# Optimization experiments

Hardware: AMD Instinct MI355X
Metric: run time of the kernel (lower is better)

Reference implementation:

```python
import jax, jax.numpy as jnp
import numpy as np

B, T, N_EMBD, HEAD = 4, 4096, 1024, 64


def setup_inputs() -> dict:
    key = jax.random.key(0)
    kx, kk, kq, kv = jax.random.split(key, 4)
    x = jax.random.normal(kx, (B, T, N_EMBD), dtype=jnp.float32)
    s = 1.0 / np.sqrt(N_EMBD)  # init scale so activations stay O(1)
    Wk = jax.random.normal(kk, (N_EMBD, HEAD), dtype=jnp.float32) * s
    Wq = jax.random.normal(kq, (N_EMBD, HEAD), dtype=jnp.float32) * s
    Wv = jax.random.normal(kv, (N_EMBD, HEAD), dtype=jnp.float32) * s
    return {"x": x, "Wk": Wk, "Wq": Wq, "Wv": Wv}


def reference(x, Wk, Wq, Wv):
    Bd, Td, C = x.shape
    k = jnp.einsum('btc,ch->bth', x, Wk)
    q = jnp.einsum('btc,ch->bth', x, Wq)
    v = jnp.einsum('btc,ch->bth', x, Wv)
    # scores scaled by C**-0.5 where C = n_embd (as in the source, not head_size)
    w = jnp.einsum('bth,bsh->bts', q, k) * (C ** -0.5)
    causal = jnp.tril(jnp.ones((Td, Td), dtype=bool))  # [T, T]
    w = jnp.where(causal, w, -jnp.inf)
    w = jax.nn.softmax(w, axis=-1)
    out = jnp.einsum('bts,bsh->bth', w, v)  # [B, T, head_size]
    return out
```

## Files before the change

### kernel.cpp

```cpp
#include <hip/hip_runtime.h>
#include <cmath>

#define NB 4
#define NT 4096
#define NC 1024
#define NH 64
#define SCALE 0.03125f
#define MFIX 3.0f
#define LOG2E 1.4426950408889634f
#define NSPLIT 12

typedef __attribute__((ext_vector_type(8))) short v8s;
typedef __attribute__((ext_vector_type(4))) float f32x4;

static __device__ __forceinline__ ushort f2bf(float x) {
    union { float f; uint u; } c; c.f = x;
    return (ushort)((c.u + 0x7FFF + ((c.u >> 16) & 1)) >> 16);
}
static __device__ __forceinline__ float bf2f(ushort h) {
    union { uint u; float f; } c; c.u = (uint)h << 16;
    return c.f;
}

__global__ __launch_bounds__(256) void prep_kernel(
    const float* __restrict__ Wk, const float* __restrict__ Wq,
    const float* __restrict__ Wv, ushort* __restrict__ Wb)
{
    const int g    = blockIdx.x * 256 + threadIdx.x;
    const int lane = g & 63;
    const int kc   = (g >> 6) & 31;
    const int nt   = g >> 11;
    const int n    = nt * 16 + (lane & 15);
    const float* W = (n < 64) ? Wq : (n < 128) ? Wk : Wv;
    const int col  = n & 63;
    const int k0   = kc * 32 + ((lane >> 4) << 3);
    ushort t8[8];
    #pragma unroll
    for (int j = 0; j < 8; ++j)
        t8[j] = f2bf(W[(k0 + j) * 64 + col]);
    *(uint4*)(Wb + (size_t)g * 8) = *(const uint4*)t8;
}

#define PPAD 72

__global__ __launch_bounds__(256) void proj_kernel(
    const float* __restrict__ x, const ushort* __restrict__ Wb,
    ushort* __restrict__ q, ushort* __restrict__ kpack, ushort* __restrict__ vpack)
{
    __shared__ __align__(16) ushort As[2][32 * PPAD];
    __shared__ __align__(16) ushort Cs[32][200];

    const int tid  = threadIdx.x;
    const int w    = tid >> 6;
    const int lane = tid & 63;
    const int ln   = lane & 15;
    const int quad = lane >> 4;
    const long r0  = (long)blockIdx.x * 32;

    const int arow = tid >> 3, acol = (tid & 7) * 8;
    const float* xs = x + (r0 + arow) * NC + acol;

    const ushort* wb0 = Wb + (size_t)(w * 3 + 0) * 16384 + lane * 8;
    const ushort* wb1 = Wb + (size_t)(w * 3 + 1) * 16384 + lane * 8;
    const ushort* wb2 = Wb + (size_t)(w * 3 + 2) * 16384 + lane * 8;

    f32x4 acc[2][3];
    #pragma unroll
    for (int s = 0; s < 2; ++s)
        #pragma unroll
        for (int nt = 0; nt < 3; ++nt) acc[s][nt] = (f32x4){0.f,0.f,0.f,0.f};

    float4 f0 = *(const float4*)(xs);
    float4 f1 = *(const float4*)(xs + 4);
    v8s b[3][2];
    b[0][0] = *(const v8s*)(wb0);       b[0][1] = *(const v8s*)(wb0 + 512);
    b[1][0] = *(const v8s*)(wb1);       b[1][1] = *(const v8s*)(wb1 + 512);
    b[2][0] = *(const v8s*)(wb2);       b[2][1] = *(const v8s*)(wb2 + 512);
    {
        ushort t8[8] = { f2bf(f0.x), f2bf(f0.y), f2bf(f0.z), f2bf(f0.w),
                         f2bf(f1.x), f2bf(f1.y), f2bf(f1.z), f2bf(f1.w) };
        *(uint4*)(&As[0][arow * PPAD + acol]) = *(const uint4*)t8;
    }
    __syncthreads();

    int buf = 0;
    #pragma unroll
    for (int it = 0; it < 16; ++it) {
        float4 g0, g1;
        v8s nb[3][2];
        if (it < 15) {
            const int k1 = (it + 1) * 64;
            g0 = *(const float4*)(xs + k1);
            g1 = *(const float4*)(xs + k1 + 4);
            const int off = (it + 1) * 1024;
            nb[0][0] = *(const v8s*)(wb0 + off); nb[0][1] = *(const v8s*)(wb0 + off + 512);
            nb[1][0] = *(const v8s*)(wb1 + off); nb[1][1] = *(const v8s*)(wb1 + off + 512);
            nb[2][0] = *(const v8s*)(wb2 + off); nb[2][1] = *(const v8s*)(wb2 + off + 512);
        }

        #pragma unroll
        for (int s = 0; s < 2; ++s) {
            const ushort* ap = &As[buf][(s * 16 + ln) * PPAD + quad * 8];
            v8s a0 = *(const v8s*)(ap);
            v8s a1 = *(const v8s*)(ap + 32);
            #pragma unroll
            for (int nt = 0; nt < 3; ++nt) {
                acc[s][nt] = __builtin_amdgcn_mfma_f32_16x16x32_bf16(a0, b[nt][0], acc[s][nt], 0, 0, 0);
                acc[s][nt] = __builtin_amdgcn_mfma_f32_16x16x32_bf16(a1, b[nt][1], acc[s][nt], 0, 0, 0);
            }
        }

        if (it < 15) {
            ushort t8[8] = { f2bf(g0.x), f2bf(g0.y), f2bf(g0.z), f2bf(g0.w),
                             f2bf(g1.x), f2bf(g1.y), f2bf(g1.z), f2bf(g1.w) };
            *(uint4*)(&As[buf ^ 1][arow * PPAD + acol]) = *(const uint4*)t8;
            #pragma unroll
            for (int nt = 0; nt < 3; ++nt) {
                b[nt][0] = nb[nt][0];
                b[nt][1] = nb[nt][1];
            }
        }
        __syncthreads();
        buf ^= 1;
    }

    #pragma unroll
    for (int s = 0; s < 2; ++s)
        #pragma unroll
        for (int nt = 0; nt < 3; ++nt)
            #pragma unroll
            for (int r = 0; r < 4; ++r)
                Cs[s * 16 + quad * 4 + r][(w * 3 + nt) * 16 + ln] = f2bf(acc[s][nt][r]);
    __syncthreads();

    const int b_blk = (int)(r0 >> 12);
    const int t_loc = (int)(r0 & 4095);
    const int kt    = t_loc >> 6;
    const int tk0   = (t_loc >> 4) & 3;
    const int kcb   = (t_loc >> 5) & 1;

    {
        const int orow = tid >> 3, oseg = (tid & 7) * 8;
        uint4 u0 = *(const uint4*)(&Cs[orow][oseg]);
        *(uint4*)(q + (r0 + orow) * NH + oseg) = u0;
    }
    {
        const int tk_loc = tid >> 7, kc = (tid >> 6) & 1, lp = tid & 63;
        const int lnp = lp & 15, qdp = lp >> 4;
        uint4 kk = *(const uint4*)(&Cs[tk_loc * 16 + lnp][64 + kc * 32 + qdp * 8]);
        size_t fid = ((size_t)(b_blk * 64 + kt) * 4 + tk0 + tk_loc) * 2 + kc;
        *(uint4*)(kpack + fid * 512 + lp * 8) = kk;
    }
    {
        const int td = tid >> 6, lp = tid & 63;
        const int lnp = lp & 15, qdp = lp >> 4;
        ushort t8[8];
        #pragma unroll
        for (int j = 0; j < 8; ++j)
            t8[j] = Cs[qdp * 8 + j][128 + td * 16 + lnp];
        size_t fid = ((size_t)(b_blk * 64 + kt) * 2 + kcb) * 4 + td;
        *(uint4*)(vpack + fid * 512 + lp * 8) = *(const uint4*)t8;
    }
}

#define LPAD 72

__global__ __launch_bounds__(256) void attn_kernel(
    const ushort* __restrict__ q, const ushort* __restrict__ kpack,
    const ushort* __restrict__ vpack, ushort* __restrict__ Op,
    float* __restrict__ Lp)
{
    __shared__ __align__(16) ushort Ps[4][32 * LPAD];

    const int id = blockIdx.x;
    const int qt = 31 - (id / 48);
    const int c  = (id % 48) >> 2;
    const int b  = id & 3;
    const int q0 = qt * 128;

    const int tid  = threadIdx.x;
    const int w    = tid >> 6;
    const int lane = tid & 63;
    const int ln   = lane & 15;
    const int quad = lane >> 4;
    const int qw0  = q0 + w * 32;

    const ushort* qb  = q + (size_t)b * NT * NH;
    const ushort* kpb = kpack + (size_t)b * 64 * 8 * 512 + lane * 8;
    const ushort* vpb = vpack + (size_t)b * 64 * 8 * 512 + lane * 8;

    v8s qf[2][2];
    #pragma unroll
    for (int s = 0; s < 2; ++s) {
        const ushort* qp = qb + (size_t)(qw0 + s * 16 + ln) * NH + quad * 8;
        qf[s][0] = *(const v8s*)(qp);
        qf[s][1] = *(const v8s*)(qp + 32);
    }

    f32x4 o[2][4];
    #pragma unroll
    for (int s = 0; s < 2; ++s)
        #pragma unroll
        for (int td = 0; td < 4; ++td) o[s][td] = (f32x4){0.f,0.f,0.f,0.f};
    float l[2][4] = {};

    const int nkt   = 2 * qt + 2;
    const int cs    = (nkt + NSPLIT - 1) / NSPLIT;
    const int kt_lo = c * cs;
    const int kt_hi = min(nkt, kt_lo + cs);

    ushort* Pw = &Ps[w][0];

    for (int kt = kt_lo; kt < kt_hi; ++kt) {
        const ushort* kfb = kpb + (size_t)kt * 8 * 512;
        const ushort* vfb = vpb + (size_t)kt * 8 * 512;

        #pragma unroll
        for (int tk = 0; tk < 4; ++tk) {
            v8s kf0 = *(const v8s*)(kfb + (tk * 2 + 0) * 512);
            v8s kf1 = *(const v8s*)(kfb + (tk * 2 + 1) * 512);
            const int sg = kt * 64 + tk * 16 + ln;
            #pragma unroll
            for (int s = 0; s < 2; ++s) {
                f32x4 acc = (f32x4){0.f,0.f,0.f,0.f};
                acc = __builtin_amdgcn_mfma_f32_16x16x32_bf16(qf[s][0], kf0, acc, 0, 0, 0);
                acc = __builtin_amdgcn_mfma_f32_16x16x32_bf16(qf[s][1], kf1, acc, 0, 0, 0);
                const bool needmask = (kt * 64 + 63) > (qw0 + s * 16);
                #pragma unroll
                for (int r = 0; r < 4; ++r) {
                    float e = fmaf(acc[r], SCALE * LOG2E, -MFIX * LOG2E);
                    if (needmask) {
                        int qg = qw0 + s * 16 + quad * 4 + r;
                        if (sg > qg) e = -1e30f;
                    }
                    float p = __builtin_amdgcn_exp2f(e);
                    l[s][r] += p;
                    Pw[(s * 16 + quad * 4 + r) * LPAD + tk * 16 + ln] = f2bf(p);
                }
            }
        }

        #pragma unroll
        for (int kc = 0; kc < 2; ++kc) {
            v8s vf[4];
            #pragma unroll
            for (int td = 0; td < 4; ++td)
                vf[td] = *(const v8s*)(vfb + (kc * 4 + td) * 512);
            #pragma unroll
            for (int s = 0; s < 2; ++s) {
                v8s pf = *(const v8s*)(&Pw[(s * 16 + ln) * LPAD + kc * 32 + quad * 8]);
                #pragma unroll
                for (int td = 0; td < 4; ++td)
                    o[s][td] = __builtin_amdgcn_mfma_f32_16x16x32_bf16(pf, vf[td], o[s][td], 0, 0, 0);
            }
        }
    }

    float lsum[2][4];
    #pragma unroll
    for (int s = 0; s < 2; ++s)
        #pragma unroll
        for (int r = 0; r < 4; ++r) {
            float x_ = l[s][r];
            x_ += __shfl_xor(x_, 1);
            x_ += __shfl_xor(x_, 2);
            x_ += __shfl_xor(x_, 4);
            x_ += __shfl_xor(x_, 8);
            lsum[s][r] = x_;
        }

    ushort* opc = Op + (size_t)c * NB * NT * NH + (size_t)b * NT * NH;
    float*  lpc = Lp + (size_t)c * NB * NT + (size_t)b * NT;
    #pragma unroll
    for (int s = 0; s < 2; ++s)
        #pragma unroll
        for (int r = 0; r < 4; ++r) {
            const int t = qw0 + s * 16 + quad * 4 + r;
            #pragma unroll
            for (int td = 0; td < 4; ++td)
                opc[(size_t)t * NH + td * 16 + ln] = f2bf(o[s][td][r]);
            if (ln == r) lpc[t] = lsum[s][r];
        }
}

__global__ __launch_bounds__(256) void combine_kernel(
    const ushort* __restrict__ Op, const float* __restrict__ Lp,
    float* __restrict__ out)
{
    const size_t g4 = (size_t)blockIdx.x * 256 + threadIdx.x;
    const size_t h0 = (g4 & 15) * 4;
    const size_t bq = g4 >> 4;
    const size_t QN = (size_t)NB * NT;
    const size_t ON = QN * NH;
    float L = 0.f;
    float o0 = 0.f, o1 = 0.f, o2 = 0.f, o3 = 0.f;
    #pragma unroll
    for (int c = 0; c < NSPLIT; ++c) {
        L += Lp[(size_t)c * QN + bq];
        ushort4 u = *(const ushort4*)(Op + (size_t)c * ON + bq * NH + h0);
        o0 += bf2f(u.x); o1 += bf2f(u.y); o2 += bf2f(u.z); o3 += bf2f(u.w);
    }
    const float inv = 1.f / L;
    float4 r = { o0 * inv, o1 * inv, o2 * inv, o3 * inv };
    *(float4*)(out + bq * NH + h0) = r;
}

extern "C" void kernel_launch(void* const* d_in, const int* in_sizes, int n_in,
                              void* d_out, int out_size, void* d_ws, size_t ws_size,
                              hipStream_t stream)
{
    const float* x  = (const float*)d_in[0];
    const float* Wk = (const float*)d_in[1];
    const float* Wq = (const float*)d_in[2];
    const float* Wv = (const float*)d_in[3];
    float* out = (float*)d_out;

    char* wsb = (char*)d_ws;
    const size_t QE = (size_t)NB * NT * NH;
    ushort* qw    = (ushort*)wsb;
    ushort* kpack = qw + QE;
    ushort* vpack = kpack + QE;
    ushort* Wb    = vpack + QE;
    ushort* Op    = (ushort*)(wsb + (8u << 20));
    float*  Lp    = (float*)(wsb + (40u << 20));

    prep_kernel<<<96, 256, 0, stream>>>(Wk, Wq, Wv, Wb);
    proj_kernel<<<NB * NT / 32, 256, 0, stream>>>(x, Wb, qw, kpack, vpack);
    attn_kernel<<<32 * NSPLIT * NB, 256, 0, stream>>>(qw, kpack, vpack, Op, Lp);
    combine_kernel<<<(int)(QE / 4 / 256), 256, 0, stream>>>(Op, Lp, out);
}
```

Before: 140.3 us.

## Transpose QK^T MFMA, pack P stores, halve projection tile, pre-pack Q

The projection kernel now handles 16 rows per block instead of 32, which doubles the grid. It writes Q in a pre-packed MFMA fragment layout so the attention kernel loads Q fragments with one contiguous load per lane. In attention, the QK^T MFMA swaps its operands so each lane holds four consecutive keys for one query. That lets the bf16 P values be packed with a perm intrinsic and stored as one 8-byte write, and the row sum needs only two cross-lane shuffles. The change targets LDS store count and shuffle overhead. The new pk2bf rounds half-up rather than round-to-nearest-even, and the proj kernel loads each B fragment twice as often per output row.

```diff
diff --git a/kernel.cpp b/kernel.cpp
--- a/kernel.cpp
+++ b/kernel.cpp
@@ -20,6 +20,11 @@
 static __device__ __forceinline__ float bf2f(ushort h) {
     union { uint u; float f; } c; c.u = (uint)h << 16;
     return c.f;
+}
+static __device__ __forceinline__ uint pk2bf(float hi_f, float lo_f) {
+    uint uh = __float_as_uint(hi_f) + 0x8000u;
+    uint ul = __float_as_uint(lo_f) + 0x8000u;
+    return __builtin_amdgcn_perm(uh, ul, 0x07060302u);
 }
 
 __global__ __launch_bounds__(256) void prep_kernel(
@@ -45,75 +50,67 @@
 
 __global__ __launch_bounds__(256) void proj_kernel(
     const float* __restrict__ x, const ushort* __restrict__ Wb,
-    ushort* __restrict__ q, ushort* __restrict__ kpack, ushort* __restrict__ vpack)
-{
-    __shared__ __align__(16) ushort As[2][32 * PPAD];
-    __shared__ __align__(16) ushort Cs[32][200];
+    ushort* __restrict__ qpack, ushort* __restrict__ kpack,
+    ushort* __restrict__ vpack)
+{
+    __shared__ __align__(16) ushort As[2][16 * PPAD];
+    __shared__ __align__(16) ushort Cs[16][200];
 
     const int tid  = threadIdx.x;
     const int w    = tid >> 6;
     const int lane = tid & 63;
     const int ln   = lane & 15;
     const int quad = lane >> 4;
-    const long r0  = (long)blockIdx.x * 32;
-
-    const int arow = tid >> 3, acol = (tid & 7) * 8;
+    const long r0  = (long)blockIdx.x * 16;
+
+    const int arow = tid >> 4, acol = (tid & 15) * 4;
     const float* xs = x + (r0 + arow) * NC + acol;
 
     const ushort* wb0 = Wb + (size_t)(w * 3 + 0) * 16384 + lane * 8;
     const ushort* wb1 = Wb + (size_t)(w * 3 + 1) * 16384 + lane * 8;
     const ushort* wb2 = Wb + (size_t)(w * 3 + 2) * 16384 + lane * 8;
 
-    f32x4 acc[2][3];
-    #pragma unroll
-    for (int s = 0; s < 2; ++s)
-        #pragma unroll
-        for (int nt = 0; nt < 3; ++nt) acc[s][nt] = (f32x4){0.f,0.f,0.f,0.f};
+    f32x4 acc[3];
+    #pragma unroll
+    for (int nt = 0; nt < 3; ++nt) acc[nt] = (f32x4){0.f,0.f,0.f,0.f};
 
     float4 f0 = *(const float4*)(xs);
-    float4 f1 = *(const float4*)(xs + 4);
     v8s b[3][2];
     b[0][0] = *(const v8s*)(wb0);       b[0][1] = *(const v8s*)(wb0 + 512);
     b[1][0] = *(const v8s*)(wb1);       b[1][1] = *(const v8s*)(wb1 + 512);
     b[2][0] = *(const v8s*)(wb2);       b[2][1] = *(const v8s*)(wb2 + 512);
     {
-        ushort t8[8] = { f2bf(f0.x), f2bf(f0.y), f2bf(f0.z), f2bf(f0.w),
-                         f2bf(f1.x), f2bf(f1.y), f2bf(f1.z), f2bf(f1.w) };
-        *(uint4*)(&As[0][arow * PPAD + acol]) = *(const uint4*)t8;
+        uint2 p = { pk2bf(f0.y, f0.x), pk2bf(f0.w, f0.z) };
+        *(uint2*)(&As[0][arow * PPAD + acol]) = p;
     }
     __syncthreads();
 
     int buf = 0;
     #pragma unroll
     for (int it = 0; it < 16; ++it) {
-        float4 g0, g1;
+        float4 g0;
         v8s nb[3][2];
         if (it < 15) {
             const int k1 = (it + 1) * 64;
             g0 = *(const float4*)(xs + k1);
-            g1 = *(const float4*)(xs + k1 + 4);
             const int off = (it + 1) * 1024;
             nb[0][0] = *(const v8s*)(wb0 + off); nb[0][1] = *(const v8s*)(wb0 + off + 512);
             nb[1][0] = *(const v8s*)(wb1 + off); nb[1][1] = *(const v8s*)(wb1 + off + 512);
             nb[2][0] = *(const v8s*)(wb2 + off); nb[2][1] = *(const v8s*)(wb2 + off + 512);
         }
 
-        #pragma unroll
-        for (int s = 0; s < 2; ++s) {
-            const ushort* ap = &As[buf][(s * 16 + ln) * PPAD + quad * 8];
-            v8s a0 = *(const v8s*)(ap);
-            v8s a1 = *(const v8s*)(ap + 32);
-            #pragma unroll
-            for (int nt = 0; nt < 3; ++nt) {
-                acc[s][nt] = __builtin_amdgcn_mfma_f32_16x16x32_bf16(a0, b[nt][0], acc[s][nt], 0, 0, 0);
-                acc[s][nt] = __builtin_amdgcn_mfma_f32_16x16x32_bf16(a1, b[nt][1], acc[s][nt], 0, 0, 0);
-            }
+        const ushort* ap = &As[buf][ln * PPAD + quad * 8];
+        v8s a0 = *(const v8s*)(ap);
+        v8s a1 = *(const v8s*)(ap + 32);
+        #pragma unroll
+        for (int nt = 0; nt < 3; ++nt) {
+            acc[nt] = __builtin_amdgcn_mfma_f32_16x16x32_bf16(a0, b[nt][0], acc[nt], 0, 0, 0);
+            acc[nt] = __builtin_amdgcn_mfma_f32_16x16x32_bf16(a1, b[nt][1], acc[nt], 0, 0, 0);
         }
 
         if (it < 15) {
-            ushort t8[8] = { f2bf(g0.x), f2bf(g0.y), f2bf(g0.z), f2bf(g0.w),
-                             f2bf(g1.x), f2bf(g1.y), f2bf(g1.z), f2bf(g1.w) };
-            *(uint4*)(&As[buf ^ 1][arow * PPAD + acol]) = *(const uint4*)t8;
+            uint2 p = { pk2bf(g0.y, g0.x), pk2bf(g0.w, g0.z) };
+            *(uint2*)(&As[buf ^ 1][arow * PPAD + acol]) = p;
             #pragma unroll
             for (int nt = 0; nt < 3; ++nt) {
                 b[nt][0] = nb[nt][0];
@@ -125,48 +122,47 @@
     }
 
     #pragma unroll
-    for (int s = 0; s < 2; ++s)
-        #pragma unroll
-        for (int nt = 0; nt < 3; ++nt)
-            #pragma unroll
-            for (int r = 0; r < 4; ++r)
-                Cs[s * 16 + quad * 4 + r][(w * 3 + nt) * 16 + ln] = f2bf(acc[s][nt][r]);
+    for (int nt = 0; nt < 3; ++nt)
+        #pragma unroll
+        for (int r = 0; r < 4; ++r)
+            Cs[quad * 4 + r][(w * 3 + nt) * 16 + ln] = f2bf(acc[nt][r]);
     __syncthreads();
 
     const int b_blk = (int)(r0 >> 12);
     const int t_loc = (int)(r0 & 4095);
     const int kt    = t_loc >> 6;
-    const int tk0   = (t_loc >> 4) & 3;
+    const int qt16  = t_loc >> 4;
     const int kcb   = (t_loc >> 5) & 1;
-
-    {
-        const int orow = tid >> 3, oseg = (tid & 7) * 8;
-        uint4 u0 = *(const uint4*)(&Cs[orow][oseg]);
-        *(uint4*)(q + (r0 + orow) * NH + oseg) = u0;
-    }
-    {
-        const int tk_loc = tid >> 7, kc = (tid >> 6) & 1, lp = tid & 63;
+    const int half  = (t_loc >> 4) & 1;
+
+    if (tid < 128) {
+        const int kc = tid >> 6, lp = tid & 63;
         const int lnp = lp & 15, qdp = lp >> 4;
-        uint4 kk = *(const uint4*)(&Cs[tk_loc * 16 + lnp][64 + kc * 32 + qdp * 8]);
-        size_t fid = ((size_t)(b_blk * 64 + kt) * 4 + tk0 + tk_loc) * 2 + kc;
-        *(uint4*)(kpack + fid * 512 + lp * 8) = kk;
-    }
-    {
-        const int td = tid >> 6, lp = tid & 63;
+        uint4 u = *(const uint4*)(&Cs[lnp][kc * 32 + qdp * 8]);
+        size_t fid = ((size_t)(b_blk * 256 + qt16) * 2 + kc);
+        *(uint4*)(qpack + fid * 512 + lp * 8) = u;
+        const int td = tid >> 5, lp2 = tid & 31;
+        const int ql = lp2 >> 4, lnv = lp2 & 15;
+        ushort t8[8];
+        #pragma unroll
+        for (int j = 0; j < 8; ++j)
+            t8[j] = Cs[ql * 8 + j][128 + td * 16 + lnv];
+        size_t fv = ((size_t)(b_blk * 64 + kt) * 2 + kcb) * 4 + td;
+        const int lane_g = (half * 2 + ql) * 16 + lnv;
+        *(uint4*)(vpack + fv * 512 + lane_g * 8) = *(const uint4*)t8;
+    } else {
+        const int kc = (tid >> 6) & 1, lp = tid & 63;
         const int lnp = lp & 15, qdp = lp >> 4;
-        ushort t8[8];
-        #pragma unroll
-        for (int j = 0; j < 8; ++j)
-            t8[j] = Cs[qdp * 8 + j][128 + td * 16 + lnp];
-        size_t fid = ((size_t)(b_blk * 64 + kt) * 2 + kcb) * 4 + td;
-        *(uint4*)(vpack + fid * 512 + lp * 8) = *(const uint4*)t8;
+        uint4 u = *(const uint4*)(&Cs[lnp][64 + kc * 32 + qdp * 8]);
+        size_t fid = ((size_t)(b_blk * 256 + qt16) * 2 + kc);
+        *(uint4*)(kpack + fid * 512 + lp * 8) = u;
     }
 }
 
 #define LPAD 72
 
 __global__ __launch_bounds__(256) void attn_kernel(
-    const ushort* __restrict__ q, const ushort* __restrict__ kpack,
+    const ushort* __restrict__ qpack, const ushort* __restrict__ kpack,
     const ushort* __restrict__ vpack, ushort* __restrict__ Op,
     float* __restrict__ Lp)
 {
@@ -184,17 +180,17 @@
     const int ln   = lane & 15;
     const int quad = lane >> 4;
     const int qw0  = q0 + w * 32;
-
-    const ushort* qb  = q + (size_t)b * NT * NH;
+    const int qt16w = (qw0 >> 4);
+
+    const ushort* qpb = qpack + (size_t)b * 256 * 2 * 512 + lane * 8;
     const ushort* kpb = kpack + (size_t)b * 64 * 8 * 512 + lane * 8;
     const ushort* vpb = vpack + (size_t)b * 64 * 8 * 512 + lane * 8;
 
     v8s qf[2][2];
     #pragma unroll
     for (int s = 0; s < 2; ++s) {
-        const ushort* qp = qb + (size_t)(qw0 + s * 16 + ln) * NH + quad * 8;
-        qf[s][0] = *(const v8s*)(qp);
-        qf[s][1] = *(const v8s*)(qp + 32);
+        qf[s][0] = *(const v8s*)(qpb + ((qt16w + s) * 2 + 0) * 512);
+        qf[s][1] = *(const v8s*)(qpb + ((qt16w + s) * 2 + 1) * 512);
     }
 
     f32x4 o[2][4];
@@ -202,7 +198,7 @@
     for (int s = 0; s < 2; ++s)
         #pragma unroll
         for (int td = 0; td < 4; ++td) o[s][td] = (f32x4){0.f,0.f,0.f,0.f};
-    float l[2][4] = {};
+    float l[2] = {0.f, 0.f};
 
     const int nkt   = 2 * qt + 2;
     const int cs    = (nkt + NSPLIT - 1) / NSPLIT;
@@ -219,24 +215,24 @@
         for (int tk = 0; tk < 4; ++tk) {
             v8s kf0 = *(const v8s*)(kfb + (tk * 2 + 0) * 512);
             v8s kf1 = *(const v8s*)(kfb + (tk * 2 + 1) * 512);
-            const int sg = kt * 64 + tk * 16 + ln;
+            const int keybase = kt * 64 + tk * 16 + quad * 4;
             #pragma unroll
             for (int s = 0; s < 2; ++s) {
                 f32x4 acc = (f32x4){0.f,0.f,0.f,0.f};
-                acc = __builtin_amdgcn_mfma_f32_16x16x32_bf16(qf[s][0], kf0, acc, 0, 0, 0);
-                acc = __builtin_amdgcn_mfma_f32_16x16x32_bf16(qf[s][1], kf1, acc, 0, 0, 0);
+                acc = __builtin_amdgcn_mfma_f32_16x16x32_bf16(kf0, qf[s][0], acc, 0, 0, 0);
+                acc = __builtin_amdgcn_mfma_f32_16x16x32_bf16(kf1, qf[s][1], acc, 0, 0, 0);
+                const int qg = qw0 + s * 16 + ln;
                 const bool needmask = (kt * 64 + 63) > (qw0 + s * 16);
+                float p[4];
                 #pragma unroll
                 for (int r = 0; r < 4; ++r) {
                     float e = fmaf(acc[r], SCALE * LOG2E, -MFIX * LOG2E);
-                    if (needmask) {
-                        int qg = qw0 + s * 16 + quad * 4 + r;
-                        if (sg > qg) e = -1e30f;
-                    }
-                    float p = __builtin_amdgcn_exp2f(e);
-                    l[s][r] += p;
-                    Pw[(s * 16 + quad * 4 + r) * LPAD + tk * 16 + ln] = f2bf(p);
+                    if (needmask && (keybase + r > qg)) e = -1e30f;
+                    p[r] = __builtin_amdgcn_exp2f(e);
+                    l[s] += p[r];
                 }
+                uint2 pw = { pk2bf(p[1], p[0]), pk2bf(p[3], p[2]) };
+                *(uint2*)(&Pw[(s * 16 + ln) * LPAD + tk * 16 + quad * 4]) = pw;
             }
         }
 
@@ -256,31 +252,25 @@
         }
     }
 
-    float lsum[2][4];
-    #pragma unroll
-    for (int s = 0; s < 2; ++s)
-        #pragma unroll
-        for (int r = 0; r < 4; ++r) {
-            float x_ = l[s][r];
-            x_ += __shfl_xor(x_, 1);
-            x_ += __shfl_xor(x_, 2);
-            x_ += __shfl_xor(x_, 4);
-            x_ += __shfl_xor(x_, 8);
-            lsum[s][r] = x_;
-        }
+    #pragma unroll
+    for (int s = 0; s < 2; ++s) {
+        l[s] += __shfl_xor(l[s], 16);
+        l[s] += __shfl_xor(l[s], 32);
+    }
 
     ushort* opc = Op + (size_t)c * NB * NT * NH + (size_t)b * NT * NH;
     float*  lpc = Lp + (size_t)c * NB * NT + (size_t)b * NT;
     #pragma unroll
-    for (int s = 0; s < 2; ++s)
+    for (int s = 0; s < 2; ++s) {
+        if (quad == 0) lpc[qw0 + s * 16 + ln] = l[s];
         #pragma unroll
         for (int r = 0; r < 4; ++r) {
             const int t = qw0 + s * 16 + quad * 4 + r;
             #pragma unroll
             for (int td = 0; td < 4; ++td)
                 opc[(size_t)t * NH + td * 16 + ln] = f2bf(o[s][td][r]);
-            if (ln == r) lpc[t] = lsum[s][r];
-        }
+        }
+    }
 }
 
 __global__ __launch_bounds__(256) void combine_kernel(
@@ -317,15 +307,15 @@
 
     char* wsb = (char*)d_ws;
     const size_t QE = (size_t)NB * NT * NH;
-    ushort* qw    = (ushort*)wsb;
-    ushort* kpack = qw + QE;
+    ushort* qpack = (ushort*)wsb;
+    ushort* kpack = qpack + QE;
     ushort* vpack = kpack + QE;
     ushort* Wb    = vpack + QE;
     ushort* Op    = (ushort*)(wsb + (8u << 20));
     float*  Lp    = (float*)(wsb + (40u << 20));
 
     prep_kernel<<<96, 256, 0, stream>>>(Wk, Wq, Wv, Wb);
-    proj_kernel<<<NB * NT / 32, 256, 0, stream>>>(x, Wb, qw, kpack, vpack);
-    attn_kernel<<<32 * NSPLIT * NB, 256, 0, stream>>>(qw, kpack, vpack, Op, Lp);
+    proj_kernel<<<NB * NT / 16, 256, 0, stream>>>(x, Wb, qpack, kpack, vpack);
+    attn_kernel<<<32 * NSPLIT * NB, 256, 0, stream>>>(qpack, kpack, vpack, Op, Lp);
     combine_kernel<<<(int)(QE / 4 / 256), 256, 0, stream>>>(Op, Lp, out);
 }
```

Measured after the change: 143.6 us. 1.02x slower.
